# Kernel tuning notes

Hardware: AMD Instinct MI355X
Metric: run time of the kernel (lower is better)

## Reference

```python
import jax, jax.numpy as jnp
import numpy as np
import math

B, Hi, Wi, D = 4, 56, 56, 256
Ho, Wo = Hi // 2, Wi // 2
HEADS, HD = D // 32, 32
NUM_ITERS, DEPTH = 3, 2
KG, KB = 3, 7
LN_EPS = 1e-5

def _ln(x, g, b):
    m = x.mean(-1, keepdims=True)
    v = ((x - m) ** 2).mean(-1, keepdims=True)
    return (x - m) * jax.lax.rsqrt(v + LN_EPS) * g + b

def _na_idx(L, K):
    # NATten neighborhood: window clamped at borders, always K neighbors
    return jnp.clip(jnp.arange(L) - K // 2, 0, L - K)[:, None] + jnp.arange(K)[None, :]

def _gather_nb(t, K):  # t [B,n,H,W,D] -> [B,n,H,K,W,K,D]
    H, W = t.shape[2], t.shape[3]
    return t[:, :, _na_idx(H, K)][:, :, :, :, _na_idx(W, K)]

def _na2d_qk(query, key, K):  # query attends to K*K neighbors of key
    b, n, H, W, d = query.shape
    return jnp.einsum('bnijd,bniajcd->bnijac', query, _gather_nb(key, K)).reshape(b, n, H, W, K * K)

def _na2d_av(attn, v, K):
    b, n, H, W, _ = attn.shape
    return jnp.einsum('bnijac,bniajcd->bnijd', attn.reshape(b, n, H, W, K, K), _gather_nb(v, K))

def _rope_cos_sin(N, hd):
    f = 1.0 / (10000.0 ** (jnp.arange(0, hd, 2, dtype=jnp.float32) / hd))
    ang = jnp.arange(N, dtype=jnp.float32)[:, None] * f[None, :]
    return jnp.cos(ang), jnp.sin(ang)

def _apply_rope(x, cos, sin):  # x [B,N,h,hd], interleaved pairs
    x2 = x.reshape(x.shape[:-1] + (-1, 2))
    x0, x1 = x2[..., 0], x2[..., 1]
    c, s = cos[None, :, None, :], sin[None, :, None, :]
    return jnp.stack([x0 * c - x1 * s, x1 * c + x0 * s], -1).reshape(x.shape)

def _forward(x, g_seed_w, g_q_w, g_k_w, g_v_w, g_mlp_w1, g_mlp_b1, g_mlp_w2, g_mlp_b2,
             g_ln_in_g, g_ln_in_b, g_ln_out_g, g_ln_out_b, g_tau, g_rpb,
             blk_ln1_g, blk_ln1_b, blk_qkv_w, blk_proj_w, blk_proj_b,
             blk_ln2_g, blk_ln2_b, blk_mlp_w1, blk_mlp_b1, blk_mlp_w2, blk_mlp_b2):
    Bx = x.shape[0]
    ln_out = lambda t: _ln(t, g_ln_out_g, g_ln_out_b)

    def to_groups(t):  # [B,N_in,D] -> [B,4,Ho,Wo,D], group p = 2*ph+pw (F.unfold 2x2 s2 order)
        m = t.reshape(Bx, Ho, 2, Wo, 2, D).transpose(0, 2, 4, 1, 3, 5)
        return m.reshape(Bx, 4, Ho, Wo, D)

    # ---- SparseGroupingLayer (local) ----
    k = to_groups(_ln(x, g_ln_in_g, g_ln_in_b) @ g_k_w.T)
    v = to_groups(x @ g_v_w.T)
    seed = jax.lax.conv_general_dilated(
        x.reshape(Bx, Hi, Wi, D), g_seed_w.transpose(2, 3, 1, 0),
        (2, 2), ((1, 1), (1, 1)), dimension_numbers=('NHWC', 'HWIO', 'NHWC'))
    x_out = ln_out(seed.reshape(Bx, Ho * Wo, D))

    ih, iw = _na_idx(Ho, KG), _na_idx(Wo, KG)
    q_idx = (ih[:, None, :, None] * Wo + iw[None, :, None, :]).reshape(-1)  # [Ho*Wo*9]
    ids_full = jnp.tile(q_idx, 4)  # same idx map for all 4 groups
    rpb = g_rpb[None, :, None, None, :]
    scale_g = jnp.exp(g_tau[0])

    for _ in range(NUM_ITERS):
        q = (ln_out(x_out) @ g_q_w.T).reshape(Bx, 1, Ho, Wo, D)
        attn = _na2d_qk(k, jnp.broadcast_to(q, (Bx, 4, Ho, Wo, D)), KG) + rpb
        attn = jax.nn.softmax(attn * scale_g, axis=-1) + 1e-6  # [B,4,Ho,Wo,9]
        col = jnp.zeros((Bx, Ho * Wo), attn.dtype).at[:, ids_full].add(attn.reshape(Bx, -1))
        denom = col[:, ids_full].reshape(Bx, 4, Ho, Wo, KG * KG)
        A_col = attn / (denom + 1e-8)
        x_out = x_out + _na2d_av(A_col, v, KG).sum(axis=1).reshape(Bx, Ho * Wo, D)
        h = jax.nn.gelu(x_out @ g_mlp_w1.T + g_mlp_b1, approximate=False) @ g_mlp_w2.T + g_mlp_b2
        x_out = x_out + ln_out(h)

    # ---- SeNaTraBlocks (local neighborhood attention, window 7, RoPE) ----
    cos, sin = _rope_cos_sin(Ho * Wo, HD)
    sc = HD ** -0.5
    for l in range(DEPTH):
        h = _ln(x_out, blk_ln1_g[l], blk_ln1_b[l])
        qkv = (h @ blk_qkv_w[l].T).reshape(Bx, Ho * Wo, 3, HEADS, HD)
        q, kk, vv = qkv[:, :, 0], qkv[:, :, 1], qkv[:, :, 2]  # [B,N,h,hd]
        q = _apply_rope(q, cos, sin).transpose(0, 2, 1, 3).reshape(Bx, HEADS, Ho, Wo, HD)
        kk = _apply_rope(kk, cos, sin).transpose(0, 2, 1, 3).reshape(Bx, HEADS, Ho, Wo, HD)
        vv = vv.transpose(0, 2, 1, 3).reshape(Bx, HEADS, Ho, Wo, HD)
        a = jax.nn.softmax(_na2d_qk(q, kk, KB) * sc, axis=-1)
        o = _na2d_av(a, vv, KB).transpose(0, 2, 3, 1, 4).reshape(Bx, Ho * Wo, D)
        x_out = x_out + (o @ blk_proj_w[l].T + blk_proj_b[l])
        h2 = _ln(x_out, blk_ln2_g[l], blk_ln2_b[l])
        m = jax.nn.gelu(h2 @ blk_mlp_w1[l].T + blk_mlp_b1[l], approximate=False) @ blk_mlp_w2[l].T + blk_mlp_b2[l]
        x_out = x_out + m
    return x_out

def setup_inputs():
    key = jax.random.key(0)
    ks = jax.random.split(key, 16)
    w = lambda k, s: jax.random.normal(k, s, dtype=jnp.float32) * 0.02
    Hm = int(D * 3.0)
    return {
        'x': jax.random.normal(ks[0], (B, Hi * Wi, D), dtype=jnp.float32),
        'g_seed_w': w(ks[1], (D, D, 3, 3)),
        'g_q_w': w(ks[2], (D, D)), 'g_k_w': w(ks[3], (D, D)), 'g_v_w': w(ks[4], (D, D)),
        'g_mlp_w1': w(ks[5], (2 * D, D)), 'g_mlp_b1': jnp.zeros((2 * D,), jnp.float32),
        'g_mlp_w2': w(ks[6], (D, 2 * D)), 'g_mlp_b2': jnp.zeros((D,), jnp.float32),
        'g_ln_in_g': jnp.ones((D,), jnp.float32), 'g_ln_in_b': jnp.zeros((D,), jnp.float32),
        'g_ln_out_g': jnp.ones((D,), jnp.float32), 'g_ln_out_b': jnp.zeros((D,), jnp.float32),
        'g_tau': jnp.full((1,), math.log(D ** -0.5), jnp.float32),
        'g_rpb': w(ks[7], (4, 9)),
        'blk_ln1_g': jnp.ones((DEPTH, D), jnp.float32), 'blk_ln1_b': jnp.zeros((DEPTH, D), jnp.float32),
        'blk_qkv_w': w(ks[8], (DEPTH, 3 * D, D)),
        'blk_proj_w': w(ks[9], (DEPTH, D, D)), 'blk_proj_b': jnp.zeros((DEPTH, D), jnp.float32),
        'blk_ln2_g': jnp.ones((DEPTH, D), jnp.float32), 'blk_ln2_b': jnp.zeros((DEPTH, D), jnp.float32),
        'blk_mlp_w1': w(ks[10], (DEPTH, Hm, D)), 'blk_mlp_b1': jnp.zeros((DEPTH, Hm), jnp.float32),
        'blk_mlp_w2': w(ks[11], (DEPTH, D, Hm)), 'blk_mlp_b2': jnp.zeros((DEPTH, D), jnp.float32),
    }

def reference(x, g_seed_w, g_q_w, g_k_w, g_v_w, g_mlp_w1, g_mlp_b1, g_mlp_w2, g_mlp_b2,
              g_ln_in_g, g_ln_in_b, g_ln_out_g, g_ln_out_b, g_tau, g_rpb,
              blk_ln1_g, blk_ln1_b, blk_qkv_w, blk_proj_w, blk_proj_b,
              blk_ln2_g, blk_ln2_b, blk_mlp_w1, blk_mlp_b1, blk_mlp_w2, blk_mlp_b2):
    return _forward(x, g_seed_w, g_q_w, g_k_w, g_v_w, g_mlp_w1, g_mlp_b1, g_mlp_w2, g_mlp_b2,
                    g_ln_in_g, g_ln_in_b, g_ln_out_g, g_ln_out_b, g_tau, g_rpb,
                    blk_ln1_g, blk_ln1_b, blk_qkv_w, blk_proj_w, blk_proj_b,
                    blk_ln2_g, blk_ln2_b, blk_mlp_w1, blk_mlp_b1, blk_mlp_w2, blk_mlp_b2)
```

## Files before the change

### kernel.cpp

```cpp
#include <hip/hip_runtime.h>
#include <hip/hip_bf16.h>
#include <math.h>

typedef __hip_bfloat16 bf16;

#define LN_EPS 1e-5f

__device__ __forceinline__ float b2f(bf16 x){ return __bfloat162float(x); }
__device__ __forceinline__ float sanit(float s){ return fminf(fmaxf(s, -80.f), 80.f); }

__device__ __forceinline__ void stc(float* p, float v){ *p = v; }
__device__ __forceinline__ void stc(bf16* p, float v){ *p = __float2bfloat16(v); }
__device__ __forceinline__ void stadd(float* p, float v){ *p += v; }
__device__ __forceinline__ void stadd(bf16* p, float v){ *p = __float2bfloat16(b2f(*p)+v); }

__device__ __forceinline__ short f2s(float f){
    union { __hip_bfloat16 h; short s; } u; u.h = __float2bfloat16(f); return u.s;
}
__device__ __forceinline__ float s2f(short s){
    union { short s; __hip_bfloat16 h; } u; u.s = s; return b2f(u.h);
}

using short8  = __attribute__((ext_vector_type(8))) short;
using floatx4 = __attribute__((ext_vector_type(4))) float;

__device__ __forceinline__ short8 load8(const float* p){
    float4 a1 = *(const float4*)p; float4 a2 = *(const float4*)(p+4);
    return (short8){ f2s(a1.x),f2s(a1.y),f2s(a1.z),f2s(a1.w),
                     f2s(a2.x),f2s(a2.y),f2s(a2.z),f2s(a2.w) };
}
__device__ __forceinline__ short8 load8(const bf16* p){ return *(const short8*)p; }

__global__ void convert_weights(const float* __restrict__ q, const float* __restrict__ k,
                                const float* __restrict__ v, const float* __restrict__ m1,
                                const float* __restrict__ m2, const float* __restrict__ qkv,
                                const float* __restrict__ proj, const float* __restrict__ bm1,
                                const float* __restrict__ bm2, bf16* __restrict__ dst)
{
    int i = blockIdx.x*256 + threadIdx.x;
    if (i >= 1769472) return;
    const float* src; int off;
    if      (i <   65536){ src=q;    off=i; }
    else if (i <  131072){ src=k;    off=i-65536; }
    else if (i <  196608){ src=v;    off=i-131072; }
    else if (i <  327680){ src=m1;   off=i-196608; }
    else if (i <  458752){ src=m2;   off=i-327680; }
    else if (i <  851968){ src=qkv;  off=i-458752; }
    else if (i <  983040){ src=proj; off=i-851968; }
    else if (i < 1376256){ src=bm1;  off=i-983040; }
    else                 { src=bm2;  off=i-1376256; }
    dst[i] = __float2bfloat16(src[off]);
}

template<typename TO>
__global__ void ln256_kernel(const float* __restrict__ in, const float* __restrict__ g,
                             const float* __restrict__ bb, TO* __restrict__ out, int addTo)
{
    int token = blockIdx.x; int d = threadIdx.x;
    int w = d >> 6, lane = d & 63;
    __shared__ float part[8];
    float v = in[(size_t)token*256 + d];
    float s = v;
    #pragma unroll
    for (int off=32; off>0; off>>=1) s += __shfl_down(s, off);
    if (lane==0) part[w] = s;
    __syncthreads();
    float mean = (part[0]+part[1]+part[2]+part[3]) * (1.f/256.f);
    float dev = v - mean;
    float q = dev*dev;
    __syncthreads();
    #pragma unroll
    for (int off=32; off>0; off>>=1) q += __shfl_down(q, off);
    if (lane==0) part[w+4] = q;
    __syncthreads();
    float var = (part[4]+part[5]+part[6]+part[7]) * (1.f/256.f);
    float r = dev*rsqrtf(var+LN_EPS)*g[d] + bb[d];
    size_t o = (size_t)token*256+d;
    if (addTo) stadd(&out[o], r); else stc(&out[o], r);
}

template<typename TA, typename TC>
__global__ __launch_bounds__(128) void gemm_mfma(const TA* __restrict__ A,
                       const bf16* __restrict__ W,
                       const float* __restrict__ bias, const float* __restrict__ resid,
                       TC* __restrict__ C, int M, int N, int K, int do_gelu)
{
    __shared__ __align__(16) short As[2][32*40];
    __shared__ __align__(16) short Ws[2][64*40];
    int t = threadIdx.x;
    int n0 = blockIdx.x*64, m0 = blockIdx.y*32;
    int lane = t & 63, w = t >> 6;
    int quad = lane >> 4, mrow = lane & 15;
    floatx4 acc[4] = {{0,0,0,0},{0,0,0,0},{0,0,0,0},{0,0,0,0}};
    int r  = t >> 2;
    int kq = (t & 3) * 8;
    const TA*   Arow  = A + (size_t)(m0 + r)*K + kq;
    const bf16* Wrow0 = W + (size_t)(n0 + r)*K + kq;
    const bf16* Wrow1 = W + (size_t)(n0 + r + 32)*K + kq;

    short8 av  = load8(Arow);
    short8 wv0 = load8(Wrow0);
    short8 wv1 = load8(Wrow1);
    *(short8*)&As[0][r*40 + kq] = av;
    *(short8*)&Ws[0][r*40 + kq] = wv0;
    *(short8*)&Ws[0][(r+32)*40 + kq] = wv1;
    __syncthreads();

    int nb = K >> 5;
    int cur = 0;
    for (int i = 0; i < nb; i++){
        if (i+1 < nb){
            int k0 = (i+1) << 5;
            av  = load8(Arow + k0);
            wv0 = load8(Wrow0 + k0);
            wv1 = load8(Wrow1 + k0);
        }
        short8 af = *(short8*)&As[cur][(w*16 + mrow)*40 + quad*8];
        #pragma unroll
        for (int nt=0; nt<4; nt++){
            short8 bfv = *(short8*)&Ws[cur][(nt*16 + mrow)*40 + quad*8];
            acc[nt] = __builtin_amdgcn_mfma_f32_16x16x32_bf16(af, bfv, acc[nt], 0, 0, 0);
        }
        if (i+1 < nb){
            int nxt = cur ^ 1;
            *(short8*)&As[nxt][r*40 + kq] = av;
            *(short8*)&Ws[nxt][r*40 + kq] = wv0;
            *(short8*)&Ws[nxt][(r+32)*40 + kq] = wv1;
            __syncthreads();
            cur = nxt;
        }
    }
    #pragma unroll
    for (int nt=0; nt<4; nt++){
        int col = n0 + nt*16 + mrow;
        float bv = bias ? bias[col] : 0.f;
        #pragma unroll
        for (int rr=0; rr<4; rr++){
            int row = m0 + w*16 + quad*4 + rr;
            float v = acc[nt][rr] + bv;
            if (do_gelu) v = 0.5f*v*(1.0f+erff(v*0.70710678118654752f));
            size_t o = (size_t)row*N + col;
            if (resid) v += resid[o];
            stc(&C[o], v);
        }
    }
}

__global__ void transpose_seedw(const float* __restrict__ w, bf16* __restrict__ wt)
{
    int idx = blockIdx.x*256 + threadIdx.x;
    if (idx >= 256*2304) return;
    int o = idx/2304; int rem = idx - o*2304; int pos = rem>>8; int ci = rem&255;
    wt[idx] = __float2bfloat16(w[(size_t)o*2304 + ci*9 + pos]);
}

__global__ __launch_bounds__(128) void conv_mfma(const float* __restrict__ x,
                       const bf16* __restrict__ wt, float* __restrict__ C)
{
    const int K = 2304, N = 256, KC = 768;
    __shared__ __align__(16) short As[2][32*40];
    __shared__ __align__(16) short Ws[2][64*40];
    int t = threadIdx.x;
    int n0 = blockIdx.x*64, m0 = blockIdx.y*32, z = blockIdx.z;
    int lane = t & 63, w = t >> 6;
    int quad = lane >> 4, mrow = lane & 15;
    floatx4 acc[4] = {{0,0,0,0},{0,0,0,0},{0,0,0,0},{0,0,0,0}};
    int r  = t >> 2;
    int kq = (t & 3) * 8;
    int m = m0 + r;
    int wo = m%28, ho = (m/28)%28, b = m/784;
    const bf16* Wrow0 = wt + (size_t)(n0 + r)*K + z*KC + kq;
    const bf16* Wrow1 = wt + (size_t)(n0 + r + 32)*K + z*KC + kq;

    int kh = z;
    int ih = 2*ho + kh - 1;
    bool rowok = (ih>=0 && ih<56);

    auto loadA = [&](int k0)->short8{
        int kk = k0 + kq;
        int pos3 = kk >> 8;
        int ci = kk & 255;
        int iw = 2*wo + pos3 - 1;
        short8 a = {0,0,0,0,0,0,0,0};
        if (rowok && iw>=0 && iw<56)
            a = load8(x + (((size_t)b*56 + ih)*56 + iw)*256 + ci);
        return a;
    };

    short8 av  = loadA(0);
    short8 wv0 = load8(Wrow0);
    short8 wv1 = load8(Wrow1);
    *(short8*)&As[0][r*40 + kq] = av;
    *(short8*)&Ws[0][r*40 + kq] = wv0;
    *(short8*)&Ws[0][(r+32)*40 + kq] = wv1;
    __syncthreads();

    const int nb = KC >> 5;
    int cur = 0;
    for (int i = 0; i < nb; i++){
        if (i+1 < nb){
            int k0 = (i+1) << 5;
            av  = loadA(k0);
            wv0 = load8(Wrow0 + k0);
            wv1 = load8(Wrow1 + k0);
        }
        short8 af = *(short8*)&As[cur][(w*16 + mrow)*40 + quad*8];
        #pragma unroll
        for (int nt=0; nt<4; nt++){
            short8 bfv = *(short8*)&Ws[cur][(nt*16 + mrow)*40 + quad*8];
            acc[nt] = __builtin_amdgcn_mfma_f32_16x16x32_bf16(af, bfv, acc[nt], 0, 0, 0);
        }
        if (i+1 < nb){
            int nxt = cur ^ 1;
            *(short8*)&As[nxt][r*40 + kq] = av;
            *(short8*)&Ws[nxt][r*40 + kq] = wv0;
            *(short8*)&Ws[nxt][(r+32)*40 + kq] = wv1;
            __syncthreads();
            cur = nxt;
        }
    }
    #pragma unroll
    for (int nt=0; nt<4; nt++){
        int col = n0 + nt*16 + mrow;
        #pragma unroll
        for (int rr=0; rr<4; rr++){
            int row = m0 + w*16 + quad*4 + rr;
            atomicAdd(&C[(size_t)row*N + col], acc[nt][rr]);
        }
    }
}

__global__ void grp_attn_kernel(const bf16* __restrict__ kproj, const bf16* __restrict__ qbuf,
                                const float* __restrict__ rpb, const float* __restrict__ g_tau,
                                float* __restrict__ attn, float* __restrict__ col)
{
    int idx = blockIdx.x;
    int j = idx%28; int i = (idx/28)%28; int n = (idx/784)%4; int b = idx/3136;
    int lane = threadIdx.x;
    int sh = n>>1, sw = n&1;
    const bf16* kv = kproj + ((size_t)b*3136 + (2*i+sh)*56 + (2*j+sw))*256;
    __shared__ float sc[9];
    __shared__ float sc2[9];
    int i0 = min(max(i-1,0),25), j0 = min(max(j-1,0),25);
    for (int l=0; l<9; l++){
        int qi = i0 + l/3, qj = j0 + l%3;
        const bf16* qv = qbuf + ((size_t)b*784 + qi*28+qj)*256;
        float p = 0.f;
        for (int d=lane; d<256; d+=64) p += b2f(kv[d])*b2f(qv[d]);
        for (int off=32; off>0; off>>=1) p += __shfl_down(p, off, 64);
        if (lane==0) sc[l] = p;
    }
    __syncthreads();
    if (lane==0){
        float scale = expf(g_tau[0]);
        float s[9]; float m = -1e30f;
        for (int l=0; l<9; l++){ s[l] = sanit((sc[l] + rpb[n*9+l])*scale); m = fmaxf(m, s[l]); }
        float sum = 0.f;
        for (int l=0; l<9; l++){ s[l] = expf(s[l]-m); sum += s[l]; }
        float inv = 1.f/fmaxf(sum, 1e-30f);
        for (int l=0; l<9; l++) sc2[l] = s[l]*inv + 1e-6f;
    }
    __syncthreads();
    if (lane < 9){
        float a = sc2[lane];
        attn[(size_t)idx*9 + lane] = a;
        int qi = i0 + lane/3, qj = j0 + lane%3;
        atomicAdd(&col[b*784 + qi*28 + qj], a);
    }
}

__global__ void grp_av_kernel(const float* __restrict__ attn, const float* __restrict__ col,
                              const bf16* __restrict__ vproj, float* __restrict__ xout)
{
    int idx = blockIdx.x;
    int j = idx%28; int i = (idx/28)%28; int b = idx/784;
    int d = threadIdx.x;
    int i0 = min(max(i-1,0),25), j0 = min(max(j-1,0),25);
    float acc = 0.f;
    for (int n=0; n<4; n++){
        int sh = n>>1, sw = n&1;
        const float* ap = attn + ((size_t)(b*4+n)*784 + i*28+j)*9;
        for (int l=0; l<9; l++){
            int qi = i0 + l/3, qj = j0 + l%3;
            float dv = col[b*784 + qi*28+qj] + 1e-8f;
            acc += (ap[l]/dv) * b2f(vproj[((size_t)b*3136 + (2*qi+sh)*56 + (2*qj+sw))*256 + d]);
        }
    }
    xout[(size_t)idx*256 + d] += acc;
}

__global__ __launch_bounds__(256) void blk_attn_row(const bf16* __restrict__ qkv,
                                                    bf16* __restrict__ obuf)
{
    int blk = blockIdx.x;
    int h = blk & 7; int rest = blk >> 3;
    int i = rest % 28; int b = rest / 28;
    int tid = threadIdx.x;
    int i0 = min(max(i-3,0),21);

    __shared__ float Ks[7*28*32];
    __shared__ float Vs[7*28*32];
    __shared__ float Qs[28*32];
    __shared__ float Ps[28*52];

    const float LOG1E4_16 = 0.5756462732485115f;

    for (int idx = tid; idx < 196*4; idx += 256){
        int pos = idx >> 2, u8 = idx & 3;
        int ki = i0 + pos/28, kj = pos - (pos/28)*28;
        int ttok = ki*28 + kj;
        const bf16* base = qkv + ((size_t)(b*784 + ttok))*768 + h*32 + u8*8;
        short8 k8 = *(const short8*)(base + 256);
        short8 v8 = *(const short8*)(base + 512);
        float f[8];
        #pragma unroll
        for (int d=0; d<8; d++) f[d] = s2f(k8[d]);
        #pragma unroll
        for (int m2=0; m2<4; m2++){
            int u = u8*4 + m2;
            float ang = (float)ttok * expf(-(float)u * LOG1E4_16);
            float c = cosf(ang), s = sinf(ang);
            float x0 = f[2*m2], x1 = f[2*m2+1];
            f[2*m2]   = x0*c - x1*s;
            f[2*m2+1] = x1*c + x0*s;
        }
        #pragma unroll
        for (int d=0; d<8; d++){
            Ks[pos*32 + u8*8 + d] = f[d];
            Vs[pos*32 + u8*8 + d] = s2f(v8[d]);
        }
    }
    for (int idx = tid; idx < 28*4; idx += 256){
        int tt = idx >> 2, u8 = idx & 3;
        int ttok = i*28 + tt;
        const bf16* base = qkv + ((size_t)(b*784 + ttok))*768 + h*32 + u8*8;
        short8 q8 = *(const short8*)base;
        float f[8];
        #pragma unroll
        for (int d=0; d<8; d++) f[d] = s2f(q8[d]);
        #pragma unroll
        for (int m2=0; m2<4; m2++){
            int u = u8*4 + m2;
            float ang = (float)ttok * expf(-(float)u * LOG1E4_16);
            float c = cosf(ang), s = sinf(ang);
            float x0 = f[2*m2], x1 = f[2*m2+1];
            f[2*m2]   = x0*c - x1*s;
            f[2*m2+1] = x1*c + x0*s;
        }
        #pragma unroll
        for (int d=0; d<8; d++) Qs[tt*32 + u8*8 + d] = f[d];
    }
    __syncthreads();

    int tt = tid >> 3, s = tid & 7;
    float sc[7];
    float mx = -1e30f;
    int j0 = min(max(tt-3,0),21);
    if (tt < 28){
        int c = 0;
        for (int l = s; l < 49; l += 8, c++){
            int ki = l/7, kj = j0 + l - (l/7)*7;
            const float4* kp = (const float4*)&Ks[(ki*28+kj)*32];
            const float4* qp = (const float4*)&Qs[tt*32];
            float p = 0.f;
            #pragma unroll
            for (int d=0; d<8; d++){
                float4 kv4 = kp[d], qv4 = qp[d];
                p += qv4.x*kv4.x + qv4.y*kv4.y + qv4.z*kv4.z + qv4.w*kv4.w;
            }
            sc[c] = sanit(p * 0.17677669529663687f);
            mx = fmaxf(mx, sc[c]);
        }
    }
    #pragma unroll
    for (int off=1; off<8; off<<=1) mx = fmaxf(mx, __shfl_xor(mx, off, 8));
    float sm = 0.f;
    if (tt < 28){
        int c = 0;
        for (int l = s; l < 49; l += 8, c++){ sc[c] = expf(sc[c]-mx); sm += sc[c]; }
    }
    #pragma unroll
    for (int off=1; off<8; off<<=1) sm += __shfl_xor(sm, off, 8);
    if (tt < 28){
        float inv = 1.f/fmaxf(sm, 1e-30f);
        int c = 0;
        for (int l = s; l < 49; l += 8, c++) Ps[tt*52 + l] = sc[c]*inv;
    }
    __syncthreads();

    for (int o = tid; o < 28*32; o += 256){
        int t2 = o >> 5, d = o & 31;
        int jj0 = min(max(t2-3,0),21);
        float acc = 0.f;
        #pragma unroll 7
        for (int l=0; l<49; l++){
            int ki = l/7, kj = jj0 + l - (l/7)*7;
            acc += Ps[t2*52 + l] * Vs[(ki*28+kj)*32 + d];
        }
        obuf[((size_t)(b*784 + i*28 + t2))*256 + h*32 + d] = __float2bfloat16(acc);
    }
}

extern "C" void kernel_launch(void* const* d_in, const int* in_sizes, int n_in,
                              void* d_out, int out_size, void* d_ws, size_t ws_size,
                              hipStream_t stream) {
    const float* x         = (const float*)d_in[0];
    const float* g_seed_w  = (const float*)d_in[1];
    const float* g_q_w     = (const float*)d_in[2];
    const float* g_k_w     = (const float*)d_in[3];
    const float* g_v_w     = (const float*)d_in[4];
    const float* g_mlp_w1  = (const float*)d_in[5];
    const float* g_mlp_b1  = (const float*)d_in[6];
    const float* g_mlp_w2  = (const float*)d_in[7];
    const float* g_mlp_b2  = (const float*)d_in[8];
    const float* g_ln_in_g = (const float*)d_in[9];
    const float* g_ln_in_b = (const float*)d_in[10];
    const float* g_ln_out_g= (const float*)d_in[11];
    const float* g_ln_out_b= (const float*)d_in[12];
    const float* g_tau     = (const float*)d_in[13];
    const float* g_rpb     = (const float*)d_in[14];
    const float* blk_ln1_g = (const float*)d_in[15];
    const float* blk_ln1_b = (const float*)d_in[16];
    const float* blk_qkv_w = (const float*)d_in[17];
    const float* blk_proj_w= (const float*)d_in[18];
    const float* blk_proj_b= (const float*)d_in[19];
    const float* blk_ln2_g = (const float*)d_in[20];
    const float* blk_ln2_b = (const float*)d_in[21];
    const float* blk_mlp_w1= (const float*)d_in[22];
    const float* blk_mlp_b1= (const float*)d_in[23];
    const float* blk_mlp_w2= (const float*)d_in[24];
    const float* blk_mlp_b2= (const float*)d_in[25];

    float* f      = (float*)d_ws;
    bf16*  wbuf   = (bf16*)d_ws;
    bf16*  kproj  = (bf16*)(f + 1179648);
    bf16*  vproj  = (bf16*)(f + 2785280);
    float* xout   = f + 4390912;
    float* tmp    = f + 5193728;
    bf16*  tmph   = (bf16*)(f + 5996544);
    bf16*  qbufh  = (bf16*)(f + 6397952);
    bf16*  bigh   = (bf16*)(f + 6799360);
    float* attng  = f + 8003584;
    float* col    = f + 8116480;
    bf16*  xln    = (bf16*)(f + 5996544);

    bf16* w_q    = wbuf;
    bf16* w_k    = wbuf + 65536;
    bf16* w_v    = wbuf + 131072;
    bf16* w_m1   = wbuf + 196608;
    bf16* w_m2   = wbuf + 327680;
    bf16* w_qkv  = wbuf + 458752;
    bf16* w_proj = wbuf + 851968;
    bf16* w_bm1  = wbuf + 983040;
    bf16* w_bm2  = wbuf + 1376256;
    bf16* w_seed = wbuf + 1769472;

    convert_weights<<<6912, 256, 0, stream>>>(g_q_w, g_k_w, g_v_w, g_mlp_w1, g_mlp_w2,
                                              blk_qkv_w, blk_proj_w, blk_mlp_w1, blk_mlp_w2, wbuf);
    transpose_seedw<<<2304, 256, 0, stream>>>(g_seed_w, w_seed);
    ln256_kernel<bf16><<<12544, 256, 0, stream>>>(x, g_ln_in_g, g_ln_in_b, xln, 0);
    gemm_mfma<bf16,bf16><<<dim3(4,392), 128, 0, stream>>>(xln, w_k, nullptr, nullptr, kproj, 12544,256,256, 0);
    gemm_mfma<float,bf16><<<dim3(4,392), 128, 0, stream>>>(x, w_v, nullptr, nullptr, vproj, 12544,256,256, 0);
    hipMemsetAsync(tmp, 0, 3136*256*sizeof(float), stream);
    conv_mfma<<<dim3(4,98,3), 128, 0, stream>>>(x, w_seed, tmp);
    ln256_kernel<float><<<3136, 256, 0, stream>>>(tmp, g_ln_out_g, g_ln_out_b, xout, 0);

    for (int it=0; it<3; it++){
        ln256_kernel<bf16><<<3136, 256, 0, stream>>>(xout, g_ln_out_g, g_ln_out_b, tmph, 0);
        gemm_mfma<bf16,bf16><<<dim3(4,98), 128, 0, stream>>>(tmph, w_q, nullptr, nullptr, qbufh, 3136,256,256, 0);
        hipMemsetAsync(col, 0, 3136*sizeof(float), stream);
        grp_attn_kernel<<<12544, 64, 0, stream>>>(kproj, qbufh, g_rpb, g_tau, attng, col);
        grp_av_kernel<<<3136, 256, 0, stream>>>(attng, col, vproj, xout);
        gemm_mfma<float,bf16><<<dim3(8,98), 128, 0, stream>>>(xout, w_m1, g_mlp_b1, nullptr, bigh, 3136,512,256, 1);
        gemm_mfma<bf16,float><<<dim3(4,98), 128, 0, stream>>>(bigh, w_m2, g_mlp_b2, nullptr, tmp, 3136,256,512, 0);
        ln256_kernel<float><<<3136, 256, 0, stream>>>(tmp, g_ln_out_g, g_ln_out_b, xout, 1);
    }

    for (int l=0; l<2; l++){
        ln256_kernel<bf16><<<3136, 256, 0, stream>>>(xout, blk_ln1_g + l*256, blk_ln1_b + l*256, tmph, 0);
        gemm_mfma<bf16,bf16><<<dim3(12,98), 128, 0, stream>>>(tmph, w_qkv + (size_t)l*196608, nullptr, nullptr, bigh, 3136,768,256, 0);
        blk_attn_row<<<896, 256, 0, stream>>>(bigh, qbufh);
        gemm_mfma<bf16,float><<<dim3(4,98), 128, 0, stream>>>(qbufh, w_proj + (size_t)l*65536, blk_proj_b + l*256, xout, xout, 3136,256,256, 0);
        ln256_kernel<bf16><<<3136, 256, 0, stream>>>(xout, blk_ln2_g + l*256, blk_ln2_b + l*256, tmph, 0);
        gemm_mfma<bf16,bf16><<<dim3(12,98), 128, 0, stream>>>(tmph, w_bm1 + (size_t)l*196608, blk_mlp_b1 + l*768, nullptr, bigh, 3136,768,256, 1);
        float* Cout = (l==1) ? (float*)d_out : xout;
        gemm_mfma<bf16,float><<<dim3(4,98), 128, 0, stream>>>(bigh, w_bm2 + (size_t)l*196608, blk_mlp_b2 + l*256, xout, Cout, 3136,256,768, 0);
    }
}
```

Baseline: 592.9 us.

## Fuse layernorms across stages, merge K/V projections, feed bf16 input to conv

```diff
diff --git a/kernel.cpp b/kernel.cpp
--- a/kernel.cpp
+++ b/kernel.cpp
@@ -79,6 +79,79 @@
     if (addTo) stadd(&out[o], r); else stc(&out[o], r);
 }
 
+__global__ void ln_cast_kernel(const float* __restrict__ in, const float* __restrict__ g,
+                               const float* __restrict__ bb, bf16* __restrict__ xln,
+                               bf16* __restrict__ xh)
+{
+    int token = blockIdx.x; int d = threadIdx.x;
+    int w = d >> 6, lane = d & 63;
+    __shared__ float part[8];
+    float v = in[(size_t)token*256 + d];
+    float s = v;
+    #pragma unroll
+    for (int off=32; off>0; off>>=1) s += __shfl_down(s, off);
+    if (lane==0) part[w] = s;
+    __syncthreads();
+    float mean = (part[0]+part[1]+part[2]+part[3]) * (1.f/256.f);
+    float dev = v - mean;
+    float q = dev*dev;
+    __syncthreads();
+    #pragma unroll
+    for (int off=32; off>0; off>>=1) q += __shfl_down(q, off);
+    if (lane==0) part[w+4] = q;
+    __syncthreads();
+    float var = (part[4]+part[5]+part[6]+part[7]) * (1.f/256.f);
+    float r = dev*rsqrtf(var+LN_EPS)*g[d] + bb[d];
+    size_t o = (size_t)token*256+d;
+    xln[o] = __float2bfloat16(r);
+    xh[o]  = __float2bfloat16(v);
+}
+
+__global__ void ln_add_ln(const float* __restrict__ in, const float* __restrict__ resid,
+                          const float* __restrict__ g1, const float* __restrict__ b1,
+                          const float* __restrict__ g2, const float* __restrict__ b2,
+                          float* __restrict__ xout, bf16* __restrict__ tmph)
+{
+    int token = blockIdx.x; int d = threadIdx.x;
+    int w = d >> 6, lane = d & 63;
+    __shared__ float part[8];
+    size_t o = (size_t)token*256 + d;
+    float v = in[o];
+    float s = v;
+    #pragma unroll
+    for (int off=32; off>0; off>>=1) s += __shfl_down(s, off);
+    if (lane==0) part[w] = s;
+    __syncthreads();
+    float mean = (part[0]+part[1]+part[2]+part[3]) * (1.f/256.f);
+    float dev = v - mean;
+    float q = dev*dev;
+    __syncthreads();
+    #pragma unroll
+    for (int off=32; off>0; off>>=1) q += __shfl_down(q, off);
+    if (lane==0) part[w+4] = q;
+    __syncthreads();
+    float var = (part[4]+part[5]+part[6]+part[7]) * (1.f/256.f);
+    float r = dev*rsqrtf(var+LN_EPS)*g1[d] + b1[d];
+    float sx = (resid ? resid[o] : 0.f) + r;
+    xout[o] = sx;
+    __syncthreads();
+    float s2 = sx;
+    #pragma unroll
+    for (int off=32; off>0; off>>=1) s2 += __shfl_down(s2, off);
+    if (lane==0) part[w] = s2;
+    __syncthreads();
+    float mean2 = (part[0]+part[1]+part[2]+part[3]) * (1.f/256.f);
+    float dev2 = sx - mean2;
+    float q2 = dev2*dev2;
+    __syncthreads();
+    #pragma unroll
+    for (int off=32; off>0; off>>=1) q2 += __shfl_down(q2, off);
+    if (lane==0) part[w+4] = q2;
+    __syncthreads();
+    float var2 = (part[4]+part[5]+part[6]+part[7]) * (1.f/256.f);
+    tmph[o] = __float2bfloat16(dev2*rsqrtf(var2+LN_EPS)*g2[d] + b2[d]);
+}
+
 template<typename TA, typename TC>
 __global__ __launch_bounds__(128) void gemm_mfma(const TA* __restrict__ A,
                        const bf16* __restrict__ W,
@@ -146,6 +219,69 @@
     }
 }
 
+__global__ __launch_bounds__(128) void gemm_kv(const bf16* __restrict__ xln,
+                       const bf16* __restrict__ xh, const bf16* __restrict__ wk,
+                       const bf16* __restrict__ wv, bf16* __restrict__ kp,
+                       bf16* __restrict__ vp)
+{
+    const int N = 256, K = 256;
+    const bf16* A = blockIdx.z ? xh : xln;
+    const bf16* W = blockIdx.z ? wv : wk;
+    bf16*       C = blockIdx.z ? vp : kp;
+    __shared__ __align__(16) short As[2][32*40];
+    __shared__ __align__(16) short Ws[2][64*40];
+    int t = threadIdx.x;
+    int n0 = blockIdx.x*64, m0 = blockIdx.y*32;
+    int lane = t & 63, w = t >> 6;
+    int quad = lane >> 4, mrow = lane & 15;
+    floatx4 acc[4] = {{0,0,0,0},{0,0,0,0},{0,0,0,0},{0,0,0,0}};
+    int r  = t >> 2;
+    int kq = (t & 3) * 8;
+    const bf16* Arow  = A + (size_t)(m0 + r)*K + kq;
+    const bf16* Wrow0 = W + (size_t)(n0 + r)*K + kq;
+    const bf16* Wrow1 = W + (size_t)(n0 + r + 32)*K + kq;
+    short8 av  = load8(Arow);
+    short8 wv0 = load8(Wrow0);
+    short8 wv1 = load8(Wrow1);
+    *(short8*)&As[0][r*40 + kq] = av;
+    *(short8*)&Ws[0][r*40 + kq] = wv0;
+    *(short8*)&Ws[0][(r+32)*40 + kq] = wv1;
+    __syncthreads();
+    const int nb = K >> 5;
+    int cur = 0;
+    for (int i = 0; i < nb; i++){
+        if (i+1 < nb){
+            int k0 = (i+1) << 5;
+            av  = load8(Arow + k0);
+            wv0 = load8(Wrow0 + k0);
+            wv1 = load8(Wrow1 + k0);
+        }
+        short8 af = *(short8*)&As[cur][(w*16 + mrow)*40 + quad*8];
+        #pragma unroll
+        for (int nt=0; nt<4; nt++){
+            short8 bfv = *(short8*)&Ws[cur][(nt*16 + mrow)*40 + quad*8];
+            acc[nt] = __builtin_amdgcn_mfma_f32_16x16x32_bf16(af, bfv, acc[nt], 0, 0, 0);
+        }
+        if (i+1 < nb){
+            int nxt = cur ^ 1;
+            *(short8*)&As[nxt][r*40 + kq] = av;
+            *(short8*)&Ws[nxt][r*40 + kq] = wv0;
+            *(short8*)&Ws[nxt][(r+32)*40 + kq] = wv1;
+            __syncthreads();
+            cur = nxt;
+        }
+    }
+    #pragma unroll
+    for (int nt=0; nt<4; nt++){
+        int col = n0 + nt*16 + mrow;
+        #pragma unroll
+        for (int rr=0; rr<4; rr++){
+            int row = m0 + w*16 + quad*4 + rr;
+            C[(size_t)row*N + col] = __float2bfloat16(acc[nt][rr]);
+        }
+    }
+}
+
 __global__ void transpose_seedw(const float* __restrict__ w, bf16* __restrict__ wt)
 {
     int idx = blockIdx.x*256 + threadIdx.x;
@@ -154,7 +290,7 @@
     wt[idx] = __float2bfloat16(w[(size_t)o*2304 + ci*9 + pos]);
 }
 
-__global__ __launch_bounds__(128) void conv_mfma(const float* __restrict__ x,
+__global__ __launch_bounds__(128) void conv_mfma(const bf16* __restrict__ xh,
                        const bf16* __restrict__ wt, float* __restrict__ C)
 {
     const int K = 2304, N = 256, KC = 768;
@@ -183,7 +319,7 @@
         int iw = 2*wo + pos3 - 1;
         short8 a = {0,0,0,0,0,0,0,0};
         if (rowok && iw>=0 && iw<56)
-            a = load8(x + (((size_t)b*56 + ih)*56 + iw)*256 + ci);
+            a = load8(xh + (((size_t)b*56 + ih)*56 + iw)*256 + ci);
         return a;
     };
 
@@ -442,7 +578,8 @@
     bf16*  bigh   = (bf16*)(f + 6799360);
     float* attng  = f + 8003584;
     float* col    = f + 8116480;
-    bf16*  xln    = (bf16*)(f + 5996544);
+    bf16*  xln    = (bf16*)(f + 8119616);
+    bf16*  xh     = (bf16*)(f + 9725248);
 
     bf16* w_q    = wbuf;
     bf16* w_k    = wbuf + 65536;
@@ -458,32 +595,37 @@
     convert_weights<<<6912, 256, 0, stream>>>(g_q_w, g_k_w, g_v_w, g_mlp_w1, g_mlp_w2,
                                               blk_qkv_w, blk_proj_w, blk_mlp_w1, blk_mlp_w2, wbuf);
     transpose_seedw<<<2304, 256, 0, stream>>>(g_seed_w, w_seed);
-    ln256_kernel<bf16><<<12544, 256, 0, stream>>>(x, g_ln_in_g, g_ln_in_b, xln, 0);
-    gemm_mfma<bf16,bf16><<<dim3(4,392), 128, 0, stream>>>(xln, w_k, nullptr, nullptr, kproj, 12544,256,256, 0);
-    gemm_mfma<float,bf16><<<dim3(4,392), 128, 0, stream>>>(x, w_v, nullptr, nullptr, vproj, 12544,256,256, 0);
+    ln_cast_kernel<<<12544, 256, 0, stream>>>(x, g_ln_in_g, g_ln_in_b, xln, xh);
+    gemm_kv<<<dim3(4,392,2), 128, 0, stream>>>(xln, xh, w_k, w_v, kproj, vproj);
     hipMemsetAsync(tmp, 0, 3136*256*sizeof(float), stream);
-    conv_mfma<<<dim3(4,98,3), 128, 0, stream>>>(x, w_seed, tmp);
-    ln256_kernel<float><<<3136, 256, 0, stream>>>(tmp, g_ln_out_g, g_ln_out_b, xout, 0);
+    conv_mfma<<<dim3(4,98,3), 128, 0, stream>>>(xh, w_seed, tmp);
+    ln_add_ln<<<3136, 256, 0, stream>>>(tmp, nullptr, g_ln_out_g, g_ln_out_b,
+                                        g_ln_out_g, g_ln_out_b, xout, tmph);
 
     for (int it=0; it<3; it++){
-        ln256_kernel<bf16><<<3136, 256, 0, stream>>>(xout, g_ln_out_g, g_ln_out_b, tmph, 0);
         gemm_mfma<bf16,bf16><<<dim3(4,98), 128, 0, stream>>>(tmph, w_q, nullptr, nullptr, qbufh, 3136,256,256, 0);
         hipMemsetAsync(col, 0, 3136*sizeof(float), stream);
         grp_attn_kernel<<<12544, 64, 0, stream>>>(kproj, qbufh, g_rpb, g_tau, attng, col);
         grp_av_kernel<<<3136, 256, 0, stream>>>(attng, col, vproj, xout);
         gemm_mfma<float,bf16><<<dim3(8,98), 128, 0, stream>>>(xout, w_m1, g_mlp_b1, nullptr, bigh, 3136,512,256, 1);
         gemm_mfma<bf16,float><<<dim3(4,98), 128, 0, stream>>>(bigh, w_m2, g_mlp_b2, nullptr, tmp, 3136,256,512, 0);
-        ln256_kernel<float><<<3136, 256, 0, stream>>>(tmp, g_ln_out_g, g_ln_out_b, xout, 1);
+        const float* g2 = (it<2) ? g_ln_out_g : blk_ln1_g;
+        const float* b2 = (it<2) ? g_ln_out_b : blk_ln1_b;
+        ln_add_ln<<<3136, 256, 0, stream>>>(tmp, xout, g_ln_out_g, g_ln_out_b,
+                                            g2, b2, xout, tmph);
     }
 
     for (int l=0; l<2; l++){
-        ln256_kernel<bf16><<<3136, 256, 0, stream>>>(xout, blk_ln1_g + l*256, blk_ln1_b + l*256, tmph, 0);
         gemm_mfma<bf16,bf16><<<dim3(12,98), 128, 0, stream>>>(tmph, w_qkv + (size_t)l*196608, nullptr, nullptr, bigh, 3136,768,256, 0);
         blk_attn_row<<<896, 256, 0, stream>>>(bigh, qbufh);
         gemm_mfma<bf16,float><<<dim3(4,98), 128, 0, stream>>>(qbufh, w_proj + (size_t)l*65536, blk_proj_b + l*256, xout, xout, 3136,256,256, 0);
         ln256_kernel<bf16><<<3136, 256, 0, stream>>>(xout, blk_ln2_g + l*256, blk_ln2_b + l*256, tmph, 0);
         gemm_mfma<bf16,bf16><<<dim3(12,98), 128, 0, stream>>>(tmph, w_bm1 + (size_t)l*196608, blk_mlp_b1 + l*768, nullptr, bigh, 3136,768,256, 1);
-        float* Cout = (l==1) ? (float*)d_out : xout;
-        gemm_mfma<bf16,float><<<dim3(4,98), 128, 0, stream>>>(bigh, w_bm2 + (size_t)l*196608, blk_mlp_b2 + l*256, xout, Cout, 3136,256,768, 0);
-    }
-}
+        if (l==0){
+            gemm_mfma<bf16,float><<<dim3(4,98), 128, 0, stream>>>(bigh, w_bm2, blk_mlp_b2, xout, xout, 3136,256,768, 0);
+            ln256_kernel<bf16><<<3136, 256, 0, stream>>>(xout, blk_ln1_g + 256, blk_ln1_b + 256, tmph, 0);
+        } else {
+            gemm_mfma<bf16,float><<<dim3(4,98), 128, 0, stream>>>(bigh, w_bm2 + 196608, blk_mlp_b2 + 256, xout, (float*)d_out, 3136,256,768, 0);
+        }
+    }
+}
```

New measurement: 573.5 us. 1.03x faster.
